# Optimization experiments

Hardware: AMD Instinct MI355X
Metric: run time of the kernel (lower is better)

The kernel has to match this reference:

```python
import jax, jax.numpy as jnp
import numpy as np

B, N, S, K, K2, C = 8, 131072, 1024, 64, 64, 32
RADIUS, RADIUS_POST = 0.4, 0.8
D1 = C + 6        # 38: mlp1 input (xyz + dim_box + feats)
H = 2 * C         # 64
D2 = H + 6        # 70: mlp2 input
H3 = 4 * H        # 256: mlp3 hidden


def _bgather(x, idx):
    # per-batch gather along axis 1 (points axis): x [B,N,...], idx [B,M] -> [B,M,...]
    return jax.vmap(lambda a, i: a[i])(x, idx)


def _conv_bn(x, w, s, t, relu=True):
    # 1x1 conv (matmul over channel) + folded eval-mode BN (scale/shift per channel)
    y = jnp.einsum('...c,cd->...d', x, w) * s + t
    return jnp.maximum(y, 0.0) if relu else y


def setup_inputs():
    key = jax.random.key(0)
    ks = jax.random.split(key, 20)
    inp = {
        'locs': jax.random.normal(ks[0], (B, N, 3), jnp.float32),
        'feats': jax.random.normal(ks[1], (B, C, N), jnp.float32),
        'boxes': jax.random.normal(ks[2], (B, N, 6), jnp.float32),
        'fps_inds': jax.random.randint(ks[3], (B, S), 0, N),
        'neighbor_inds': jax.random.randint(ks[4], (B, S * K), 0, N),
        'neighbor_inds2': jax.random.randint(ks[5], (B, S * K2), 0, S),
    }
    def w(k, i, o):
        return jax.random.normal(k, (i, o), jnp.float32) * (1.0 / np.sqrt(i))
    def bn(k, c):
        k1, k2 = jax.random.split(k)
        return (1.0 + 0.1 * jax.random.normal(k1, (c,), jnp.float32),
                0.1 * jax.random.normal(k2, (c,), jnp.float32))
    inp['w1a'] = w(ks[6], D1, C);  inp['s1a'], inp['t1a'] = bn(ks[7], C)
    inp['w1b'] = w(ks[8], C, H);   inp['s1b'], inp['t1b'] = bn(ks[9], H)
    inp['w2'] = w(ks[10], D2, H);  inp['s2'], inp['t2'] = bn(ks[11], H)
    inp['w3a'] = w(ks[12], H, H3); inp['s3a'], inp['t3a'] = bn(ks[13], H3)
    inp['w3b'] = w(ks[14], H3, H); inp['s3b'], inp['t3b'] = bn(ks[15], H)
    return inp


def reference(locs, feats, boxes, fps_inds, neighbor_inds, neighbor_inds2,
              w1a, s1a, t1a, w1b, s1b, t1b, w2, s2, t2,
              w3a, s3a, t3a, w3b, s3b, t3b):
    feats_nc = jnp.transpose(feats, (0, 2, 1))          # [B,N,C]
    dim_boxes = boxes[..., 3:] - boxes[..., :3]          # [B,N,3]

    fps_locs = _bgather(locs, fps_inds)                  # [B,S,3]
    fps_dim = _bgather(dim_boxes, fps_inds)              # [B,S,3]
    fps_boxes = _bgather(boxes, fps_inds)                # [B,S,6]

    # --- stage 1: ball-query gather on raw points ---
    gxyz = _bgather(locs, neighbor_inds).reshape(B, S, K, 3)
    gxyz = (gxyz - fps_locs[:, :, None, :]) / RADIUS
    gdim = _bgather(dim_boxes, neighbor_inds).reshape(B, S, K, 3)
    gdim = jnp.abs(gdim - fps_dim[:, :, None, :])
    gfeat = _bgather(feats_nc, neighbor_inds).reshape(B, S, K, C)
    g = jnp.concatenate([gxyz, gdim, gfeat], axis=-1)    # [B,S,K,38]

    h = _conv_bn(g, w1a, s1a, t1a, relu=True)
    h = _conv_bn(h, w1b, s1b, t1b, relu=True)            # [B,S,K,64]
    new_features = jnp.max(h, axis=2)                    # [B,S,64]
    identity = new_features

    # --- stage 2: ball-query gather on FPS points ---
    gxyz2 = _bgather(fps_locs, neighbor_inds2).reshape(B, S, K2, 3)
    gxyz2 = (gxyz2 - fps_locs[:, :, None, :]) / RADIUS_POST
    gdim2 = _bgather(fps_dim, neighbor_inds2).reshape(B, S, K2, 3)
    gdim2 = jnp.abs(gdim2 - fps_dim[:, :, None, :])
    gfeat2 = _bgather(new_features, neighbor_inds2).reshape(B, S, K2, H)
    g2 = jnp.concatenate([gxyz2, gdim2, gfeat2], axis=-1)  # [B,S,K2,70]

    h2 = _conv_bn(g2, w2, s2, t2, relu=False)            # [B,S,K2,64]
    h2 = jnp.max(h2, axis=2)                             # [B,S,64]

    # --- mlp_module3 (Conv1d bottleneck) + skip ---
    h3 = _conv_bn(h2, w3a, s3a, t3a, relu=True)          # [B,S,256]
    h3 = _conv_bn(h3, w3b, s3b, t3b, relu=False)         # [B,S,64]
    out = jnp.maximum(h3 + identity, 0.0)                # skip_act

    return fps_locs, jnp.transpose(out, (0, 2, 1)), fps_boxes, fps_inds
```

## Files before the change

kernel.cpp:

```cpp
#include <hip/hip_runtime.h>
#include <hip/hip_bf16.h>
#include <stdint.h>

#define DEV __device__ __forceinline__

constexpr int B_ = 8, N_ = 131072, S_ = 1024, C_ = 32;
constexpr float INV_R1 = 2.5f;
constexpr float INV_R2 = 1.25f;

constexpr int OW1AS = 0;
constexpr int OW1BS = 1216;
constexpr int OT1B  = 3264;
constexpr int OW2S  = 3328;
constexpr int OT2   = 7808;
constexpr int OW3AS = 7872;
constexpr int OT3A  = 24256;
constexpr int OW3BS = 24512;
constexpr int OT3B  = 40896;

constexpr size_t WS_CTR  = 163840;
constexpr size_t WS_NF   = WS_CTR  + (size_t)8192*104*4;
constexpr size_t WS_P2   = WS_NF   + (size_t)524288*4;
constexpr size_t WS_HOUT = WS_P2   + (size_t)524288*4;
constexpr size_t WS_PREC = WS_HOUT + (size_t)524288*4;

DEV float bfu(uint16_t u){ return __uint_as_float(((uint32_t)u) << 16); }

__global__ void k_weights(
    const float* __restrict__ w1a, const float* __restrict__ s1a,
    const float* __restrict__ w1b, const float* __restrict__ s1b,
    const float* __restrict__ t1b,
    const float* __restrict__ w2,  const float* __restrict__ s2,
    const float* __restrict__ t2,
    const float* __restrict__ w3a, const float* __restrict__ s3a,
    const float* __restrict__ t3a,
    const float* __restrict__ w3b, const float* __restrict__ s3b,
    const float* __restrict__ t3b,
    float* __restrict__ wsw)
{
  int t = blockIdx.x*256 + threadIdx.x;
  int nth = gridDim.x*256;
  for (int i=t;i<38*32;i+=nth)  wsw[OW1AS+i] = w1a[i]*s1a[i&31];
  for (int i=t;i<32*64;i+=nth)  wsw[OW1BS+i] = w1b[i]*s1b[i&63];
  for (int i=t;i<64;i+=nth)     wsw[OT1B+i]  = t1b[i];
  for (int i=t;i<70*64;i+=nth)  wsw[OW2S+i]  = w2[i]*s2[i&63];
  for (int i=t;i<64;i+=nth)     wsw[OT2+i]   = t2[i];
  for (int i=t;i<64*256;i+=nth) wsw[OW3AS+i] = w3a[i]*s3a[i&255];
  for (int i=t;i<256;i+=nth)    wsw[OT3A+i]  = t3a[i];
  for (int i=t;i<256*64;i+=nth) wsw[OW3BS+i] = w3b[i]*s3b[i&63];
  for (int i=t;i<64;i+=nth)     wsw[OT3B+i]  = t3b[i];
}

__global__ __launch_bounds__(256) void k_points(
    const float* __restrict__ locs,
    const float* __restrict__ feats,
    const float* __restrict__ wsw,
    __hip_bfloat16* __restrict__ prec)
{
  size_t p = (size_t)blockIdx.x*256 + threadIdx.x;
  int b = (int)(p >> 17);
  int pinb = (int)(p & (size_t)(N_-1));

  float x = locs[p*3+0]*INV_R1;
  float y = locs[p*3+1]*INV_R1;
  float z = locs[p*3+2]*INV_R1;

  float acc[32];
  #pragma unroll
  for (int j=0;j<32;j++)
    acc[j] = x*wsw[OW1AS+j] + y*wsw[OW1AS+32+j] + z*wsw[OW1AS+64+j];

  const float* fb = feats + (size_t)b*C_*N_ + pinb;
  #pragma unroll
  for (int c=0;c<32;c++){
    float f = fb[(size_t)c*N_];
    #pragma unroll
    for (int j=0;j<32;j++)
      acc[j] = fmaf(f, wsw[OW1AS + (6+c)*32 + j], acc[j]);
  }
  union U { float4 v[4]; __hip_bfloat16 h[32]; } r;
  #pragma unroll
  for (int j=0;j<32;j++) r.h[j] = __float2bfloat16(acc[j]);
  float4* dst = (float4*)(prec + p*32);
  dst[0]=r.v[0]; dst[1]=r.v[1]; dst[2]=r.v[2]; dst[3]=r.v[3];
}

__global__ __launch_bounds__(256) void k_centers(
    const float* __restrict__ locs,
    const float* __restrict__ boxes,
    const int* __restrict__ fps_inds,
    const float* __restrict__ t1a,
    const float* __restrict__ wsw,
    float* __restrict__ ctr,
    float* __restrict__ out0,
    float* __restrict__ out2,
    float* __restrict__ out3)
{
  int i = blockIdx.x*256 + threadIdx.x;
  int b = i >> 10;
  int idx = fps_inds[i];
  size_t src = (size_t)b*N_ + (uint32_t)idx;

  float x = locs[src*3+0], y = locs[src*3+1], z = locs[src*3+2];
  out0[(size_t)i*3+0]=x; out0[(size_t)i*3+1]=y; out0[(size_t)i*3+2]=z;
  float bx0=boxes[src*6+0], bx1=boxes[src*6+1], bx2=boxes[src*6+2];
  float bx3=boxes[src*6+3], bx4=boxes[src*6+4], bx5=boxes[src*6+5];
  out2[(size_t)i*6+0]=bx0; out2[(size_t)i*6+1]=bx1; out2[(size_t)i*6+2]=bx2;
  out2[(size_t)i*6+3]=bx3; out2[(size_t)i*6+4]=bx4; out2[(size_t)i*6+5]=bx5;
  out3[i] = (float)idx;

  float d0=bx3-bx0, d1=bx4-bx1, d2=bx5-bx2;
  float* cr = ctr + (size_t)i*104;
  cr[0]=x; cr[1]=y; cr[2]=z; cr[3]=d0; cr[4]=d1; cr[5]=d2; cr[6]=0.f; cr[7]=0.f;
  float xr=x*INV_R1, yr=y*INV_R1, zr=z*INV_R1;
  #pragma unroll
  for (int j=0;j<32;j++)
    cr[8+j] = t1a[j] - xr*wsw[OW1AS+j] - yr*wsw[OW1AS+32+j] - zr*wsw[OW1AS+64+j];
  float xq=x*INV_R2, yq=y*INV_R2, zq=z*INV_R2;
  #pragma unroll
  for (int j=0;j<64;j++)
    cr[40+j] = wsw[OT2+j] - xq*wsw[OW2S+j] - yq*wsw[OW2S+64+j] - zq*wsw[OW2S+128+j];
}

__global__ __launch_bounds__(256) void k_stage1(
    const float* __restrict__ boxes,
    const int* __restrict__ neighbor_inds,
    const __hip_bfloat16* __restrict__ prec,
    const float* __restrict__ wsw,
    const float* __restrict__ ctr,
    float* __restrict__ nf,
    float* __restrict__ p2)
{
  int wid  = (blockIdx.x*256 + threadIdx.x) >> 6;
  int lane = threadIdx.x & 63;
  int uwid = __builtin_amdgcn_readfirstlane(wid);
  int b = uwid >> 10;

  int nbr = neighbor_inds[(size_t)uwid*64 + lane];
  size_t gp = (size_t)b*N_ + (uint32_t)nbr;

  union U { float4 v[4]; uint16_t u[32]; } r;
  const float4* psrc = (const float4*)(prec + gp*32);
  r.v[0]=psrc[0]; r.v[1]=psrc[1]; r.v[2]=psrc[2]; r.v[3]=psrc[3];

  const float2* bp = (const float2*)(boxes + gp*6);
  float2 q0=bp[0], q1=bp[1], q2=bp[2];

  const float* cr = ctr + (size_t)uwid*104;
  float ad0=fabsf((q1.y-q0.x)-cr[3]);
  float ad1=fabsf((q2.x-q0.y)-cr[4]);
  float ad2=fabsf((q2.y-q1.x)-cr[5]);

  float h[32];
  #pragma unroll
  for (int i=0;i<32;i++){
    float p = bfu(r.u[i]);
    float v = p + cr[8+i] + ad0*wsw[OW1AS+96+i] + ad1*wsw[OW1AS+128+i] + ad2*wsw[OW1AS+160+i];
    h[i] = fmaxf(v, 0.f);
  }
  float acc[64];
  #pragma unroll
  for (int j=0;j<64;j++) acc[j] = wsw[OT1B+j];
  #pragma unroll
  for (int i=0;i<32;i++){
    #pragma unroll
    for (int j=0;j<64;j++)
      acc[j] = fmaf(h[i], wsw[OW1BS + i*64 + j], acc[j]);
  }
  float mine = 0.f;
  #pragma unroll
  for (int j=0;j<64;j++){
    float m = acc[j];
    m = fmaxf(m, __shfl_xor(m, 1));
    m = fmaxf(m, __shfl_xor(m, 2));
    m = fmaxf(m, __shfl_xor(m, 4));
    m = fmaxf(m, __shfl_xor(m, 8));
    m = fmaxf(m, __shfl_xor(m, 16));
    m = fmaxf(m, __shfl_xor(m, 32));
    m = fmaxf(m, 0.f);
    acc[j] = m;
    mine = (lane == j) ? m : mine;
  }
  nf[(size_t)uwid*64 + lane] = mine;

  float pv = (cr[0]*INV_R2)*wsw[OW2S+lane]
           + (cr[1]*INV_R2)*wsw[OW2S+64+lane]
           + (cr[2]*INV_R2)*wsw[OW2S+128+lane];
  #pragma unroll
  for (int i=0;i<64;i++)
    pv = fmaf(acc[i], wsw[OW2S + (6+i)*64 + lane], pv);
  p2[(size_t)uwid*64 + lane] = pv;
}

__global__ __launch_bounds__(256) void k_stage23(
    const int* __restrict__ ninds2,
    const float* __restrict__ wsw,
    const float* __restrict__ ctr,
    const float* __restrict__ nf,
    const float* __restrict__ p2,
    float* __restrict__ hout)
{
  int wid  = (blockIdx.x*256 + threadIdx.x) >> 6;
  int lane = threadIdx.x & 63;
  int uwid = __builtin_amdgcn_readfirstlane(wid);
  int bS = uwid & ~1023;

  const float* cr = ctr + (size_t)uwid*104;
  float q2  = cr[40+lane];
  float cd0 = cr[3], cd1 = cr[4], cd2 = cr[5];
  float w30 = wsw[OW2S+192+lane];
  float w31 = wsw[OW2S+256+lane];
  float w32 = wsw[OW2S+320+lane];

  const int* nix = ninds2 + (size_t)uwid*64;
  float m = -3.4e38f;
  #pragma unroll 8
  for (int k=0;k<64;k++){
    int nb = nix[k];
    int g  = bS + nb;
    const float* ncr = ctr + (size_t)g*104;
    float a0 = fabsf(ncr[3]-cd0);
    float a1 = fabsf(ncr[4]-cd1);
    float a2 = fabsf(ncr[5]-cd2);
    float v = p2[(size_t)g*64 + lane] + q2 + a0*w30 + a1*w31 + a2*w32;
    m = fmaxf(m, v);
  }

  float h3[4];
  #pragma unroll
  for (int t=0;t<4;t++) h3[t] = wsw[OT3A + t*64 + lane];
  #pragma unroll
  for (int i=0;i<64;i++){
    float h2i = __shfl(m, i);
    #pragma unroll
    for (int t=0;t<4;t++)
      h3[t] = fmaf(h2i, wsw[OW3AS + i*256 + t*64 + lane], h3[t]);
  }
  #pragma unroll
  for (int t=0;t<4;t++) h3[t] = fmaxf(h3[t], 0.f);

  float o = wsw[OT3B + lane];
  #pragma unroll
  for (int t=0;t<4;t++){
    #pragma unroll
    for (int l=0;l<64;l++){
      float v = __shfl(h3[t], l);
      o = fmaf(v, wsw[OW3BS + (t*64+l)*64 + lane], o);
    }
  }
  float idv = nf[(size_t)uwid*64 + lane];
  o = fmaxf(o + idv, 0.f);
  hout[(size_t)uwid*64 + lane] = o;
}

__global__ __launch_bounds__(256) void k_transpose(
    const float* __restrict__ hout, float* __restrict__ out1)
{
  __shared__ float tile[64][65];
  int bb = blockIdx.x >> 4;
  int s0 = (blockIdx.x & 15) << 6;
  int c  = threadIdx.x & 63;
  int r4 = threadIdx.x >> 6;
  #pragma unroll
  for (int r=0;r<16;r++){
    int sr = r*4 + r4;
    tile[sr][c] = hout[((size_t)bb*S_ + s0 + sr)*64 + c];
  }
  __syncthreads();
  #pragma unroll
  for (int r=0;r<16;r++){
    int j = r*4 + r4;
    out1[(size_t)bb*64*S_ + (size_t)j*S_ + s0 + c] = tile[c][j];
  }
}

extern "C" void kernel_launch(void* const* d_in, const int* in_sizes, int n_in,
                              void* d_out, int out_size, void* d_ws, size_t ws_size,
                              hipStream_t stream) {
  const float* locs  = (const float*)d_in[0];
  const float* feats = (const float*)d_in[1];
  const float* boxes = (const float*)d_in[2];
  const int* fps_inds = (const int*)d_in[3];
  const int* ninds    = (const int*)d_in[4];
  const int* ninds2   = (const int*)d_in[5];
  const float* w1a=(const float*)d_in[6];
  const float* s1a=(const float*)d_in[7];
  const float* t1a=(const float*)d_in[8];
  const float* w1b=(const float*)d_in[9];
  const float* s1b=(const float*)d_in[10];
  const float* t1b=(const float*)d_in[11];
  const float* w2 =(const float*)d_in[12];
  const float* s2 =(const float*)d_in[13];
  const float* t2 =(const float*)d_in[14];
  const float* w3a=(const float*)d_in[15];
  const float* s3a=(const float*)d_in[16];
  const float* t3a=(const float*)d_in[17];
  const float* w3b=(const float*)d_in[18];
  const float* s3b=(const float*)d_in[19];
  const float* t3b=(const float*)d_in[20];

  float* wsw  = (float*)d_ws;
  float* ctr  = (float*)((char*)d_ws + WS_CTR);
  float* nf   = (float*)((char*)d_ws + WS_NF);
  float* p2b  = (float*)((char*)d_ws + WS_P2);
  float* hout = (float*)((char*)d_ws + WS_HOUT);
  __hip_bfloat16* prec = (__hip_bfloat16*)((char*)d_ws + WS_PREC);

  float* out  = (float*)d_out;
  float* out0 = out;
  float* out1 = out + 24576;
  float* out2 = out + 548864;
  float* out3 = out + 598016;

  k_weights<<<160, 256, 0, stream>>>(w1a,s1a,w1b,s1b,t1b,w2,s2,t2,w3a,s3a,t3a,w3b,s3b,t3b,wsw);
  k_points<<<4096, 256, 0, stream>>>(locs, feats, wsw, prec);
  k_centers<<<32, 256, 0, stream>>>(locs, boxes, fps_inds, t1a, wsw, ctr, out0, out2, out3);
  k_stage1<<<2048, 256, 0, stream>>>(boxes, ninds, prec, wsw, ctr, nf, p2b);
  k_stage23<<<2048, 256, 0, stream>>>(ninds2, wsw, ctr, nf, p2b, hout);
  k_transpose<<<128, 256, 0, stream>>>(hout, out1);
}
```

Baseline: 409.5 us.

## Process two points per thread, four centers per wave, and use butterfly max-reduce

k_points now handles two points per thread with vectorized float2 loads, so each weight load is shared across both points and the grid is halved. k_stage1 replaces 64 independent six-step shuffle reductions with a butterfly transpose-reduce that needs far fewer shuffles, then rebroadcasts the results with __shfl for the mlp2 projection. k_stage23 processes four centers per wave so each weight load from mlp3 is reused four times, and the grid is cut to a quarter. The cost is higher register pressure and possibly lower occupancy.

```diff
diff --git a/kernel.cpp b/kernel.cpp
--- a/kernel.cpp
+++ b/kernel.cpp
@@ -57,32 +57,40 @@
     const float* __restrict__ wsw,
     __hip_bfloat16* __restrict__ prec)
 {
-  size_t p = (size_t)blockIdx.x*256 + threadIdx.x;
-  int b = (int)(p >> 17);
-  int pinb = (int)(p & (size_t)(N_-1));
-
-  float x = locs[p*3+0]*INV_R1;
-  float y = locs[p*3+1]*INV_R1;
-  float z = locs[p*3+2]*INV_R1;
-
-  float acc[32];
-  #pragma unroll
-  for (int j=0;j<32;j++)
-    acc[j] = x*wsw[OW1AS+j] + y*wsw[OW1AS+32+j] + z*wsw[OW1AS+64+j];
-
+  size_t t = (size_t)blockIdx.x*256 + threadIdx.x;
+  size_t p0 = t*2;
+  int b = (int)(p0 >> 17);
+  int pinb = (int)(p0 & (size_t)(N_-1));
+
+  const float2* lp = (const float2*)(locs + p0*3);
+  float2 a0=lp[0], a1=lp[1], a2=lp[2];
+  float x0=a0.x*INV_R1, y0=a0.y*INV_R1, z0=a1.x*INV_R1;
+  float x1=a1.y*INV_R1, y1=a2.x*INV_R1, z1=a2.y*INV_R1;
+
+  float acc0[32], acc1[32];
+  #pragma unroll
+  for (int j=0;j<32;j++){
+    float wa=wsw[OW1AS+j], wb=wsw[OW1AS+32+j], wc=wsw[OW1AS+64+j];
+    acc0[j] = x0*wa + y0*wb + z0*wc;
+    acc1[j] = x1*wa + y1*wb + z1*wc;
+  }
   const float* fb = feats + (size_t)b*C_*N_ + pinb;
   #pragma unroll
   for (int c=0;c<32;c++){
-    float f = fb[(size_t)c*N_];
-    #pragma unroll
-    for (int j=0;j<32;j++)
-      acc[j] = fmaf(f, wsw[OW1AS + (6+c)*32 + j], acc[j]);
-  }
-  union U { float4 v[4]; __hip_bfloat16 h[32]; } r;
-  #pragma unroll
-  for (int j=0;j<32;j++) r.h[j] = __float2bfloat16(acc[j]);
-  float4* dst = (float4*)(prec + p*32);
-  dst[0]=r.v[0]; dst[1]=r.v[1]; dst[2]=r.v[2]; dst[3]=r.v[3];
+    float2 f = *(const float2*)(fb + (size_t)c*N_);
+    #pragma unroll
+    for (int j=0;j<32;j++){
+      float w = wsw[OW1AS + (6+c)*32 + j];
+      acc0[j] = fmaf(f.x, w, acc0[j]);
+      acc1[j] = fmaf(f.y, w, acc1[j]);
+    }
+  }
+  union U { float4 v[4]; __hip_bfloat16 h[32]; } r0, r1;
+  #pragma unroll
+  for (int j=0;j<32;j++){ r0.h[j]=__float2bfloat16(acc0[j]); r1.h[j]=__float2bfloat16(acc1[j]); }
+  float4* dst = (float4*)(prec + p0*32);
+  dst[0]=r0.v[0]; dst[1]=r0.v[1]; dst[2]=r0.v[2]; dst[3]=r0.v[3];
+  dst[4]=r1.v[0]; dst[5]=r1.v[1]; dst[6]=r1.v[2]; dst[7]=r1.v[3];
 }
 
 __global__ __launch_bounds__(256) void k_centers(
@@ -167,20 +175,17 @@
     for (int j=0;j<64;j++)
       acc[j] = fmaf(h[i], wsw[OW1BS + i*64 + j], acc[j]);
   }
-  float mine = 0.f;
-  #pragma unroll
-  for (int j=0;j<64;j++){
-    float m = acc[j];
-    m = fmaxf(m, __shfl_xor(m, 1));
-    m = fmaxf(m, __shfl_xor(m, 2));
-    m = fmaxf(m, __shfl_xor(m, 4));
-    m = fmaxf(m, __shfl_xor(m, 8));
-    m = fmaxf(m, __shfl_xor(m, 16));
-    m = fmaxf(m, __shfl_xor(m, 32));
-    m = fmaxf(m, 0.f);
-    acc[j] = m;
-    mine = (lane == j) ? m : mine;
-  }
+  #pragma unroll
+  for (int s=32;s>=1;s>>=1){
+    bool up = (lane & s) != 0;
+    #pragma unroll
+    for (int i=0;i<s;i++){
+      float lo = fmaxf(acc[i],   __shfl_xor(acc[i],   s));
+      float hi = fmaxf(acc[s+i], __shfl_xor(acc[s+i], s));
+      acc[i] = up ? hi : lo;
+    }
+  }
+  float mine = fmaxf(acc[0], 0.f);
   nf[(size_t)uwid*64 + lane] = mine;
 
   float pv = (cr[0]*INV_R2)*wsw[OW2S+lane]
@@ -188,7 +193,7 @@
            + (cr[2]*INV_R2)*wsw[OW2S+128+lane];
   #pragma unroll
   for (int i=0;i<64;i++)
-    pv = fmaf(acc[i], wsw[OW2S + (6+i)*64 + lane], pv);
+    pv = fmaf(__shfl(mine, i), wsw[OW2S + (6+i)*64 + lane], pv);
   p2[(size_t)uwid*64 + lane] = pv;
 }
 
@@ -202,55 +207,80 @@
 {
   int wid  = (blockIdx.x*256 + threadIdx.x) >> 6;
   int lane = threadIdx.x & 63;
-  int uwid = __builtin_amdgcn_readfirstlane(wid);
-  int bS = uwid & ~1023;
-
-  const float* cr = ctr + (size_t)uwid*104;
-  float q2  = cr[40+lane];
-  float cd0 = cr[3], cd1 = cr[4], cd2 = cr[5];
+  int uw = __builtin_amdgcn_readfirstlane(wid);
+  int c0 = uw*4;
+  int bS = c0 & ~1023;
+
+  float q2v[4], m[4], cd0[4], cd1[4], cd2[4];
+  #pragma unroll
+  for (int g=0;g<4;g++){
+    const float* cr = ctr + (size_t)(c0+g)*104;
+    q2v[g] = cr[40+lane];
+    cd0[g]=cr[3]; cd1[g]=cr[4]; cd2[g]=cr[5];
+    m[g] = -3.4e38f;
+  }
   float w30 = wsw[OW2S+192+lane];
   float w31 = wsw[OW2S+256+lane];
   float w32 = wsw[OW2S+320+lane];
 
-  const int* nix = ninds2 + (size_t)uwid*64;
-  float m = -3.4e38f;
+  #pragma unroll 4
+  for (int k=0;k<64;k++){
+    #pragma unroll
+    for (int g=0;g<4;g++){
+      int nb = ninds2[(size_t)(c0+g)*64 + k];
+      int gg = bS + nb;
+      const float* ncr = ctr + (size_t)gg*104;
+      float a0 = fabsf(ncr[3]-cd0[g]);
+      float a1 = fabsf(ncr[4]-cd1[g]);
+      float a2 = fabsf(ncr[5]-cd2[g]);
+      float v = p2[(size_t)gg*64 + lane] + q2v[g] + a0*w30 + a1*w31 + a2*w32;
+      m[g] = fmaxf(m[g], v);
+    }
+  }
+
+  float h3[4][4];
+  #pragma unroll
+  for (int g=0;g<4;g++)
+    #pragma unroll
+    for (int t=0;t<4;t++) h3[g][t] = wsw[OT3A + t*64 + lane];
   #pragma unroll 8
-  for (int k=0;k<64;k++){
-    int nb = nix[k];
-    int g  = bS + nb;
-    const float* ncr = ctr + (size_t)g*104;
-    float a0 = fabsf(ncr[3]-cd0);
-    float a1 = fabsf(ncr[4]-cd1);
-    float a2 = fabsf(ncr[5]-cd2);
-    float v = p2[(size_t)g*64 + lane] + q2 + a0*w30 + a1*w31 + a2*w32;
-    m = fmaxf(m, v);
-  }
-
-  float h3[4];
-  #pragma unroll
-  for (int t=0;t<4;t++) h3[t] = wsw[OT3A + t*64 + lane];
-  #pragma unroll
   for (int i=0;i<64;i++){
-    float h2i = __shfl(m, i);
-    #pragma unroll
-    for (int t=0;t<4;t++)
-      h3[t] = fmaf(h2i, wsw[OW3AS + i*256 + t*64 + lane], h3[t]);
-  }
-  #pragma unroll
-  for (int t=0;t<4;t++) h3[t] = fmaxf(h3[t], 0.f);
-
-  float o = wsw[OT3B + lane];
+    float wv0 = wsw[OW3AS + i*256 +   0 + lane];
+    float wv1 = wsw[OW3AS + i*256 +  64 + lane];
+    float wv2 = wsw[OW3AS + i*256 + 128 + lane];
+    float wv3 = wsw[OW3AS + i*256 + 192 + lane];
+    #pragma unroll
+    for (int g=0;g<4;g++){
+      float h2i = __shfl(m[g], i);
+      h3[g][0] = fmaf(h2i, wv0, h3[g][0]);
+      h3[g][1] = fmaf(h2i, wv1, h3[g][1]);
+      h3[g][2] = fmaf(h2i, wv2, h3[g][2]);
+      h3[g][3] = fmaf(h2i, wv3, h3[g][3]);
+    }
+  }
+  #pragma unroll
+  for (int g=0;g<4;g++)
+    #pragma unroll
+    for (int t=0;t<4;t++) h3[g][t] = fmaxf(h3[g][t], 0.f);
+
+  float o[4];
+  #pragma unroll
+  for (int g=0;g<4;g++) o[g] = wsw[OT3B + lane];
   #pragma unroll
   for (int t=0;t<4;t++){
-    #pragma unroll
+    #pragma unroll 8
     for (int l=0;l<64;l++){
-      float v = __shfl(h3[t], l);
-      o = fmaf(v, wsw[OW3BS + (t*64+l)*64 + lane], o);
-    }
-  }
-  float idv = nf[(size_t)uwid*64 + lane];
-  o = fmaxf(o + idv, 0.f);
-  hout[(size_t)uwid*64 + lane] = o;
+      float wb = wsw[OW3BS + (t*64+l)*64 + lane];
+      #pragma unroll
+      for (int g=0;g<4;g++)
+        o[g] = fmaf(__shfl(h3[g][t], l), wb, o[g]);
+    }
+  }
+  #pragma unroll
+  for (int g=0;g<4;g++){
+    float idv = nf[(size_t)(c0+g)*64 + lane];
+    hout[(size_t)(c0+g)*64 + lane] = fmaxf(o[g] + idv, 0.f);
+  }
 }
 
 __global__ __launch_bounds__(256) void k_transpose(
@@ -313,9 +343,9 @@
   float* out3 = out + 598016;
 
   k_weights<<<160, 256, 0, stream>>>(w1a,s1a,w1b,s1b,t1b,w2,s2,t2,w3a,s3a,t3a,w3b,s3b,t3b,wsw);
-  k_points<<<4096, 256, 0, stream>>>(locs, feats, wsw, prec);
+  k_points<<<2048, 256, 0, stream>>>(locs, feats, wsw, prec);
   k_centers<<<32, 256, 0, stream>>>(locs, boxes, fps_inds, t1a, wsw, ctr, out0, out2, out3);
   k_stage1<<<2048, 256, 0, stream>>>(boxes, ninds, prec, wsw, ctr, nf, p2b);
-  k_stage23<<<2048, 256, 0, stream>>>(ninds2, wsw, ctr, nf, p2b, hout);
+  k_stage23<<<512, 256, 0, stream>>>(ninds2, wsw, ctr, nf, p2b, hout);
   k_transpose<<<128, 256, 0, stream>>>(hout, out1);
 }
```

Result: slower. 866.7 us (+111.7%).
